# Performance work log

Measured on AMD Instinct MI355X. Metric: run time of the kernel, lower is better.

The kernel has to match this reference:

```python
import jax, jax.numpy as jnp
import numpy as np

# MX microscaling decode helpers. Codes are stored as int32 holding uint8 bit patterns.
_FP4_MAG = jnp.array([0.0, 0.5, 1.0, 1.5, 2.0, 3.0, 4.0, 6.0], dtype=jnp.float32)  # E2M1

def dec_fp4(c):
    # c in [0,16): bit3 = sign, bits0-2 index E2M1 magnitude LUT
    s = jnp.where(c >= 8, -1.0, 1.0)
    return s * _FP4_MAG[c & 7]

def dec_fp6(c):
    # E3M2, bias 3. bit5 sign, bits2-4 exp, bits0-1 mantissa
    s = jnp.where(c >= 32, -1.0, 1.0)
    e = ((c >> 2) & 7).astype(jnp.float32)
    m = (c & 3).astype(jnp.float32)
    mag = jnp.where(e == 0, m * 0.25 * 0.25, (1.0 + m * 0.25) * jnp.exp2(e - 3.0))
    return s * mag

def dec_fp8(c):
    # E4M3, bias 7. bit7 sign, bits3-6 exp, bits0-2 mantissa (NaN code decoded as 480, consistent both sides)
    s = jnp.where(c >= 128, -1.0, 1.0)
    e = ((c >> 3) & 15).astype(jnp.float32)
    m = (c & 7).astype(jnp.float32)
    mag = jnp.where(e == 0, m * 0.125 * jnp.exp2(-6.0), (1.0 + m * 0.125) * jnp.exp2(e - 7.0))
    return s * mag

def unpack4(p):
    # [..., K//2] bytes -> [..., K] nibbles; low nibble = even element, high = odd
    lo = p & 15
    hi = (p >> 4) & 15
    return jnp.stack([lo, hi], axis=-1).reshape(*p.shape[:-1], p.shape[-1] * 2)

def unpack6(p):
    # little-endian 6-bit packing: 4 values per 3 bytes. [..., K*6//8] -> [..., K]
    g = p.reshape(*p.shape[:-1], -1, 3)
    b0, b1, b2 = g[..., 0], g[..., 1], g[..., 2]
    v0 = b0 & 0x3F
    v1 = ((b0 >> 6) & 3) | ((b1 & 0x0F) << 2)
    v2 = ((b1 >> 4) & 0x0F) | ((b2 & 3) << 4)
    v3 = (b2 >> 2) & 0x3F
    return jnp.stack([v0, v1, v2, v3], axis=-1).reshape(*p.shape[:-1], p.shape[-1] * 4 // 3)

def blockscale(x, sf):
    # x [..., K] fp32, sf [..., K//32] E8M0 exponents: scale = 2^(sf-127) per 32-element block
    scale = jnp.exp2(sf.astype(jnp.float32) - 127.0)
    xs = x.reshape(*x.shape[:-1], -1, 32) * scale[..., None]
    return xs.reshape(x.shape)

def dequant(codes, sf, bits):
    if bits == 4:
        x = dec_fp4(unpack4(codes))
    elif bits == 6:
        x = dec_fp6(unpack6(codes))
    else:
        x = dec_fp8(codes)
    return blockscale(x, sf)


def setup_inputs() -> dict:
    key = jax.random.key(0)
    ks = jax.random.split(key, 13)
    M, N = 4096, 4096
    p4, p6, p8 = 3072, 768, 256
    ri = lambda k, sh: jax.random.randint(k, sh, 0, 256, dtype=jnp.int32)
    sf = lambda k, sh: jax.random.randint(k, sh, 121, 132, dtype=jnp.int32)
    return {
        "AN": ri(ks[0], (M, p4 // 2)),
        "AS": ri(ks[1], (M, p6 * 6 // 8)),
        "AO": ri(ks[2], (M, p8)),
        "SFAN": sf(ks[3], (M, p4 // 32)),
        "SFAS": sf(ks[4], (M, p6 // 32)),
        "SFAO": sf(ks[5], (M, p8 // 32)),
        "BN": ri(ks[6], (N, p4 // 2)),
        "BS": ri(ks[7], (N, p6 * 6 // 8)),
        "BO": ri(ks[8], (N, p8)),
        "SFBN": sf(ks[9], (N * p4 // 32,)),
        "SFBS": sf(ks[10], (N * p6 // 32,)),
        "SFBO": sf(ks[11], (N * p8 // 32,)),
        "bias": jax.random.normal(ks[12], (N,), dtype=jnp.float32) * 0.02,
    }


def reference(AN, AS, AO, SFAN, SFAS, SFAO, BN, BS, BO, SFBN, SFBS, SFBO, bias):
    N = BN.shape[0]
    a4 = dequant(AN, SFAN, 4)                       # [M, p4]
    w4 = dequant(BN, SFBN.reshape(N, -1), 4)        # [N, p4]
    a6 = dequant(AS, SFAS, 6)                       # [M, p6]
    w6 = dequant(BS, SFBS.reshape(N, -1), 6)        # [N, p6]
    a8 = dequant(AO, SFAO, 8)                       # [M, p8]
    w8 = dequant(BO, SFBO.reshape(N, -1), 8)        # [N, p8]
    y = a4 @ w4.T + a6 @ w6.T + a8 @ w8.T           # [M, N]
    return y + bias
```

## Files before the change

### kernel.cpp

```cpp
#include <hip/hip_runtime.h>

typedef short short8 __attribute__((ext_vector_type(8)));
typedef int   intx8  __attribute__((ext_vector_type(8)));
typedef float floatx16 __attribute__((ext_vector_type(16)));

__device__ __forceinline__ unsigned short f2bf(float f) {
    union { float f; unsigned u; } v; v.f = f;
    unsigned r = (v.u + 0x7FFF + ((v.u >> 16) & 1)) >> 16;
    return (unsigned short)r;
}
__device__ __forceinline__ float dec8f(int c) {
    float s = (c & 128) ? -1.f : 1.f;
    int e = (c >> 3) & 15, m = c & 7;
    float mag = e ? ldexpf(1.f + 0.125f * (float)m, e - 7) : ldexpf(0.125f * (float)m, -6);
    return s * mag;
}
__device__ __forceinline__ unsigned pk4(int a, int b, int c, int d) {
    return (a & 255) | ((b & 255) << 8) | ((c & 255) << 16) | ((unsigned)(d & 255) << 24);
}

__global__ __launch_bounds__(256) void pack_side(
    const int* __restrict__ Pn, const int* __restrict__ Ps, const int* __restrict__ Po,
    const int* __restrict__ Sn, const int* __restrict__ Ss, const int* __restrict__ So,
    unsigned char* __restrict__ C4, unsigned char* __restrict__ C6,
    unsigned short* __restrict__ C8, unsigned char* __restrict__ St, int R)
{
    int t = blockIdx.x * 256 + threadIdx.x;
    int T0 = R * 96, T1 = T0 + R * 24, T2 = T1 + R * 32, T3 = T2 + R * 24, T4 = T3 + R * 12;
    if (t < T0) {
        int j = t / R, r = t - j * R;
        const int4* p = (const int4*)(Pn + (size_t)r * 1536 + j * 16);
        uint4 o; unsigned* po = (unsigned*)&o;
        #pragma unroll
        for (int q = 0; q < 4; q++) { int4 b = p[q]; po[q] = pk4(b.x, b.y, b.z, b.w); }
        *(uint4*)(C4 + ((size_t)j * R + r) * 16) = o;
    } else if (t < T1) {
        t -= T0; int g = t / R, r = t - g * R;
        const int4* p = (const int4*)(Ps + (size_t)r * 576 + g * 24);
        unsigned d[6];
        #pragma unroll
        for (int q = 0; q < 6; q++) { int4 b = p[q]; d[q] = pk4(b.x, b.y, b.z, b.w); }
        unsigned char* dst = C6 + ((size_t)g * R + r) * 24;
        *(int2*)(dst)      = (int2){ (int)d[0], (int)d[1] };
        *(int2*)(dst + 8)  = (int2){ (int)d[2], (int)d[3] };
        *(int2*)(dst + 16) = (int2){ (int)d[4], (int)d[5] };
    } else if (t < T2) {
        t -= T1; int j = t / R, r = t - j * R;
        const int4* p = (const int4*)(Po + (size_t)r * 256 + j * 8);
        int4 c0 = p[0], c1 = p[1];
        int e = So[r * 8 + (j >> 2)] - 127;
        int cs[8] = { c0.x, c0.y, c0.z, c0.w, c1.x, c1.y, c1.z, c1.w };
        uint4 o; unsigned* po = (unsigned*)&o;
        #pragma unroll
        for (int i = 0; i < 4; i++) {
            unsigned lo = f2bf(ldexpf(dec8f(cs[2 * i] & 255), e));
            unsigned hi = f2bf(ldexpf(dec8f(cs[2 * i + 1] & 255), e));
            po[i] = lo | (hi << 16);
        }
        *(uint4*)((unsigned char*)C8 + ((size_t)j * R + r) * 16) = o;
    } else if (t < T3) {
        t -= T2; int q = t / R, r = t - q * R;
        int4 v = *(const int4*)(Sn + (size_t)r * 96 + q * 4);
        *(unsigned*)(St + ((size_t)q * R + r) * 4) = pk4(v.x, v.y, v.z, v.w);
    } else if (t < T4) {
        t -= T3; int b2 = t / R, r = t - b2 * R;
        int s0 = Ss[(size_t)r * 24 + 2 * b2] & 255, s1 = Ss[(size_t)r * 24 + 2 * b2 + 1] & 255;
        *(unsigned*)(St + ((size_t)(24 + b2) * R + r) * 4) = (unsigned)(s0 | (s1 << 8));
    }
}

__global__ __launch_bounds__(256, 2) void gemm_mx(
    const unsigned char* __restrict__ A4, const unsigned char* __restrict__ B4,
    const unsigned char* __restrict__ A6, const unsigned char* __restrict__ B6,
    const unsigned short* __restrict__ A8, const unsigned short* __restrict__ B8,
    const unsigned char* __restrict__ SaT, const unsigned char* __restrict__ SbT,
    const float* __restrict__ bias, float* __restrict__ C, int M, int N)
{
    int tid = threadIdx.x, w = tid >> 6, l = tid & 63;
    int bm = blockIdx.y, bn = blockIdx.x;
    int wm = (w >> 1) * 64, wn = (w & 1) * 64;
    int lr = l & 31, lh = l >> 5;

    floatx16 acc[2][2] = {};

    int rA[2] = { bm * 128 + wm + lr, bm * 128 + wm + 32 + lr };
    int cB[2] = { bn * 128 + wn + lr, bn * 128 + wn + 32 + lr };

    {
        unsigned offA[2] = { ((unsigned)lh * M + rA[0]) * 16u, ((unsigned)lh * M + rA[1]) * 16u };
        unsigned offB[2] = { ((unsigned)lh * N + cB[0]) * 16u, ((unsigned)lh * N + cB[1]) * 16u };
        unsigned strA = 32u * (unsigned)M, strB = 32u * (unsigned)N;
        #pragma unroll 2
        for (int up = 0; up < 24; ++up) {
            unsigned sca0 = *(const unsigned*)(SaT + ((size_t)up * M + rA[0]) * 4);
            unsigned sca1 = *(const unsigned*)(SaT + ((size_t)up * M + rA[1]) * 4);
            unsigned scb0 = *(const unsigned*)(SbT + ((size_t)up * N + cB[0]) * 4);
            unsigned scb1 = *(const unsigned*)(SbT + ((size_t)up * N + cB[1]) * 4);
            #pragma unroll
            for (int s = 0; s < 2; ++s) {
                unsigned u = (unsigned)(up * 2 + s);
                intx8 af[2], bfr[2];
                #pragma unroll
                for (int i = 0; i < 2; i++) {
                    int4 v = *(const int4*)(A4 + offA[i] + (size_t)u * strA);
                    af[i] = (intx8){ v.x, v.y, v.z, v.w, 0, 0, 0, 0 };
                }
                #pragma unroll
                for (int j = 0; j < 2; j++) {
                    int4 v = *(const int4*)(B4 + offB[j] + (size_t)u * strB);
                    bfr[j] = (intx8){ v.x, v.y, v.z, v.w, 0, 0, 0, 0 };
                }
                int sh = 8 * (s * 2 + lh);
                int sa[2] = { (int)((sca0 >> sh) & 255), (int)((sca1 >> sh) & 255) };
                int sb[2] = { (int)((scb0 >> sh) & 255), (int)((scb1 >> sh) & 255) };
                #pragma unroll
                for (int i = 0; i < 2; i++)
                    #pragma unroll
                    for (int j = 0; j < 2; j++)
                        acc[i][j] = __builtin_amdgcn_mfma_scale_f32_32x32x64_f8f6f4(
                            af[i], bfr[j], acc[i][j], 4, 4, 0, sa[i], 0, sb[j]);
            }
        }
    }

    {
        #pragma unroll 2
        for (int v = 0; v < 12; ++v) {
            unsigned sca0 = *(const unsigned*)(SaT + ((size_t)(24 + v) * M + rA[0]) * 4);
            unsigned sca1 = *(const unsigned*)(SaT + ((size_t)(24 + v) * M + rA[1]) * 4);
            unsigned scb0 = *(const unsigned*)(SbT + ((size_t)(24 + v) * N + cB[0]) * 4);
            unsigned scb1 = *(const unsigned*)(SbT + ((size_t)(24 + v) * N + cB[1]) * 4);
            intx8 af[2], bfr[2];
            #pragma unroll
            for (int i = 0; i < 2; i++) {
                const unsigned char* p = A6 + ((size_t)(2 * v + lh) * M + rA[i]) * 24;
                int2 u0 = *(const int2*)(p), u1 = *(const int2*)(p + 8), u2 = *(const int2*)(p + 16);
                af[i] = (intx8){ u0.x, u0.y, u1.x, u1.y, u2.x, u2.y, 0, 0 };
            }
            #pragma unroll
            for (int j = 0; j < 2; j++) {
                const unsigned char* p = B6 + ((size_t)(2 * v + lh) * N + cB[j]) * 24;
                int2 u0 = *(const int2*)(p), u1 = *(const int2*)(p + 8), u2 = *(const int2*)(p + 16);
                bfr[j] = (intx8){ u0.x, u0.y, u1.x, u1.y, u2.x, u2.y, 0, 0 };
            }
            int sh = 8 * lh;
            int sa[2] = { (int)((sca0 >> sh) & 255), (int)((sca1 >> sh) & 255) };
            int sb[2] = { (int)((scb0 >> sh) & 255), (int)((scb1 >> sh) & 255) };
            #pragma unroll
            for (int i = 0; i < 2; i++)
                #pragma unroll
                for (int j = 0; j < 2; j++)
                    acc[i][j] = __builtin_amdgcn_mfma_scale_f32_32x32x64_f8f6f4(
                        af[i], bfr[j], acc[i][j], 3, 3, 0, sa[i], 0, sb[j]);
        }
    }

    {
        #pragma unroll 2
        for (int q = 0; q < 16; ++q) {
            short8 af[2], bfr[2];
            #pragma unroll
            for (int i = 0; i < 2; i++)
                af[i] = *(const short8*)(A8 + ((size_t)(2 * q + lh) * M + rA[i]) * 8);
            #pragma unroll
            for (int j = 0; j < 2; j++)
                bfr[j] = *(const short8*)(B8 + ((size_t)(2 * q + lh) * N + cB[j]) * 8);
            #pragma unroll
            for (int i = 0; i < 2; i++)
                #pragma unroll
                for (int j = 0; j < 2; j++)
                    acc[i][j] = __builtin_amdgcn_mfma_f32_32x32x16_bf16(af[i], bfr[j], acc[i][j], 0, 0, 0);
        }
    }

    #pragma unroll
    for (int i = 0; i < 2; i++)
        #pragma unroll
        for (int j = 0; j < 2; j++) {
            int col = bn * 128 + wn + j * 32 + lr;
            float bv = bias[col];
            #pragma unroll
            for (int r = 0; r < 16; r++) {
                int row = bm * 128 + wm + i * 32 + (r & 3) + 8 * (r >> 2) + 4 * lh;
                C[(size_t)row * N + col] = acc[i][j][r] + bv;
            }
        }
}

extern "C" void kernel_launch(void* const* d_in, const int* in_sizes, int n_in,
                              void* d_out, int out_size, void* d_ws, size_t ws_size,
                              hipStream_t stream) {
    const int* AN   = (const int*)d_in[0];
    const int* ASs  = (const int*)d_in[1];
    const int* AO   = (const int*)d_in[2];
    const int* SFAN = (const int*)d_in[3];
    const int* SFAS = (const int*)d_in[4];
    const int* SFAO = (const int*)d_in[5];
    const int* BN   = (const int*)d_in[6];
    const int* BS   = (const int*)d_in[7];
    const int* BO   = (const int*)d_in[8];
    const int* SFBN = (const int*)d_in[9];
    const int* SFBS = (const int*)d_in[10];
    const int* SFBO = (const int*)d_in[11];
    const float* bias = (const float*)d_in[12];

    int M = in_sizes[0] / 1536;
    int N = in_sizes[6] / 1536;

    unsigned char* ws = (unsigned char*)d_ws;
    size_t o = 0;
    unsigned char*  A4c = ws + o;                    o += (size_t)M * 1536;
    unsigned char*  B4c = ws + o;                    o += (size_t)N * 1536;
    unsigned char*  A6c = ws + o;                    o += (size_t)M * 576;
    unsigned char*  B6c = ws + o;                    o += (size_t)N * 576;
    unsigned short* A8d = (unsigned short*)(ws + o); o += (size_t)M * 512;
    unsigned short* B8d = (unsigned short*)(ws + o); o += (size_t)N * 512;
    unsigned char*  SaT = ws + o;                    o += (size_t)36 * M * 4;
    unsigned char*  SbT = ws + o;                    o += (size_t)36 * N * 4;

    int TA = M * 188, TB = N * 188;
    pack_side<<<(TA + 255) / 256, 256, 0, stream>>>(AN, ASs, AO, SFAN, SFAS, SFAO,
                                                    A4c, A6c, A8d, SaT, M);
    pack_side<<<(TB + 255) / 256, 256, 0, stream>>>(BN, BS, BO, SFBN, SFBS, SFBO,
                                                    B4c, B6c, B8d, SbT, N);

    dim3 grid(N / 128, M / 128);
    gemm_mx<<<grid, 256, 0, stream>>>(A4c, B4c, A6c, B6c, A8d, B8d,
                                      SaT, SbT, bias, (float*)d_out, M, N);
}
```

Measured before the change: 227.6 us.

## Merge pack kernels, use integer fp8-to-bf16 decode, register-prefetch GEMM operands

The two pack launches are merged into one kernel, and each pack thread now handles more work. The fp8 decode to bf16 is rewritten as integer bit manipulation instead of float ldexp plus rounding. In the GEMM, every section (fp4, fp6, bf16) gets register double or quad buffering of operand fragments and scales, so global loads for later steps are issued before the current MFMAs run. This is meant to hide load latency in a kernel that does no LDS staging, at the cost of higher register pressure. That pressure could limit occupancy under launch_bounds(256,2).

New measurement: 209.9 us. 1.08x faster.

```diff
diff --git a/kernel.cpp b/kernel.cpp
--- a/kernel.cpp
+++ b/kernel.cpp
@@ -4,36 +4,36 @@
 typedef int   intx8  __attribute__((ext_vector_type(8)));
 typedef float floatx16 __attribute__((ext_vector_type(16)));
 
-__device__ __forceinline__ unsigned short f2bf(float f) {
-    union { float f; unsigned u; } v; v.f = f;
-    unsigned r = (v.u + 0x7FFF + ((v.u >> 16) & 1)) >> 16;
-    return (unsigned short)r;
-}
-__device__ __forceinline__ float dec8f(int c) {
-    float s = (c & 128) ? -1.f : 1.f;
-    int e = (c >> 3) & 15, m = c & 7;
-    float mag = e ? ldexpf(1.f + 0.125f * (float)m, e - 7) : ldexpf(0.125f * (float)m, -6);
-    return s * mag;
-}
 __device__ __forceinline__ unsigned pk4(int a, int b, int c, int d) {
     return (a & 255) | ((b & 255) << 8) | ((c & 255) << 16) | ((unsigned)(d & 255) << 24);
 }
 
-__global__ __launch_bounds__(256) void pack_side(
-    const int* __restrict__ Pn, const int* __restrict__ Ps, const int* __restrict__ Po,
+__device__ __forceinline__ unsigned dec8bf(int c, int esf) {
+    int s = (c & 128) << 8;
+    int e = (c >> 3) & 15, m = c & 7;
+    int rn = s | ((e + 120 + esf) << 7) | (m << 4);
+    int nb = (m >= 4) ? 2 : ((m >= 2) ? 1 : 0);
+    int rs = m ? (s | ((nb + 118 + esf) << 7) | ((m << (7 - nb)) & 0x7F)) : s;
+    return (unsigned)(e ? rn : rs);
+}
+
+__device__ __forceinline__ void pack_one(
+    int t, const int* __restrict__ Pn, const int* __restrict__ Ps, const int* __restrict__ Po,
     const int* __restrict__ Sn, const int* __restrict__ Ss, const int* __restrict__ So,
     unsigned char* __restrict__ C4, unsigned char* __restrict__ C6,
     unsigned short* __restrict__ C8, unsigned char* __restrict__ St, int R)
 {
-    int t = blockIdx.x * 256 + threadIdx.x;
-    int T0 = R * 96, T1 = T0 + R * 24, T2 = T1 + R * 32, T3 = T2 + R * 24, T4 = T3 + R * 12;
+    int T0 = R * 48, T1 = T0 + R * 24, T2 = T1 + R * 8, T3 = T2 + R * 24, T4 = T3 + R * 12;
     if (t < T0) {
-        int j = t / R, r = t - j * R;
-        const int4* p = (const int4*)(Pn + (size_t)r * 1536 + j * 16);
-        uint4 o; unsigned* po = (unsigned*)&o;
-        #pragma unroll
-        for (int q = 0; q < 4; q++) { int4 b = p[q]; po[q] = pk4(b.x, b.y, b.z, b.w); }
-        *(uint4*)(C4 + ((size_t)j * R + r) * 16) = o;
+        int jj = t / R, r = t - jj * R;
+        const int4* p = (const int4*)(Pn + (size_t)r * 1536 + jj * 32);
+        #pragma unroll
+        for (int h = 0; h < 2; ++h) {
+            uint4 o; unsigned* po = (unsigned*)&o;
+            #pragma unroll
+            for (int q = 0; q < 4; q++) { int4 b = p[4 * h + q]; po[q] = pk4(b.x, b.y, b.z, b.w); }
+            *(uint4*)(C4 + ((size_t)(2 * jj + h) * R + r) * 16) = o;
+        }
     } else if (t < T1) {
         t -= T0; int g = t / R, r = t - g * R;
         const int4* p = (const int4*)(Ps + (size_t)r * 576 + g * 24);
@@ -45,19 +45,19 @@
         *(int2*)(dst + 8)  = (int2){ (int)d[2], (int)d[3] };
         *(int2*)(dst + 16) = (int2){ (int)d[4], (int)d[5] };
     } else if (t < T2) {
-        t -= T1; int j = t / R, r = t - j * R;
-        const int4* p = (const int4*)(Po + (size_t)r * 256 + j * 8);
-        int4 c0 = p[0], c1 = p[1];
-        int e = So[r * 8 + (j >> 2)] - 127;
-        int cs[8] = { c0.x, c0.y, c0.z, c0.w, c1.x, c1.y, c1.z, c1.w };
-        uint4 o; unsigned* po = (unsigned*)&o;
-        #pragma unroll
-        for (int i = 0; i < 4; i++) {
-            unsigned lo = f2bf(ldexpf(dec8f(cs[2 * i] & 255), e));
-            unsigned hi = f2bf(ldexpf(dec8f(cs[2 * i + 1] & 255), e));
-            po[i] = lo | (hi << 16);
-        }
-        *(uint4*)((unsigned char*)C8 + ((size_t)j * R + r) * 16) = o;
+        t -= T1; int jj = t / R, r = t - jj * R;
+        const int4* p = (const int4*)(Po + (size_t)r * 256 + jj * 32);
+        int e = So[r * 8 + jj] - 127;
+        #pragma unroll
+        for (int cq = 0; cq < 4; ++cq) {
+            int4 c0 = p[2 * cq], c1 = p[2 * cq + 1];
+            int cs[8] = { c0.x, c0.y, c0.z, c0.w, c1.x, c1.y, c1.z, c1.w };
+            uint4 o; unsigned* po = (unsigned*)&o;
+            #pragma unroll
+            for (int i = 0; i < 4; i++)
+                po[i] = dec8bf(cs[2 * i] & 255, e) | (dec8bf(cs[2 * i + 1] & 255, e) << 16);
+            *(uint4*)((unsigned char*)C8 + ((size_t)(4 * jj + cq) * R + r) * 16) = o;
+        }
     } else if (t < T3) {
         t -= T2; int q = t / R, r = t - q * R;
         int4 v = *(const int4*)(Sn + (size_t)r * 96 + q * 4);
@@ -67,6 +67,22 @@
         int s0 = Ss[(size_t)r * 24 + 2 * b2] & 255, s1 = Ss[(size_t)r * 24 + 2 * b2 + 1] & 255;
         *(unsigned*)(St + ((size_t)(24 + b2) * R + r) * 4) = (unsigned)(s0 | (s1 << 8));
     }
+}
+
+__global__ __launch_bounds__(256) void pack_both(
+    const int* __restrict__ AN, const int* __restrict__ AS, const int* __restrict__ AO,
+    const int* __restrict__ SAn, const int* __restrict__ SAs, const int* __restrict__ SAo,
+    unsigned char* __restrict__ A4, unsigned char* __restrict__ A6,
+    unsigned short* __restrict__ A8, unsigned char* __restrict__ SaT, int M,
+    const int* __restrict__ BN, const int* __restrict__ BS, const int* __restrict__ BO,
+    const int* __restrict__ SBn, const int* __restrict__ SBs, const int* __restrict__ SBo,
+    unsigned char* __restrict__ B4, unsigned char* __restrict__ B6,
+    unsigned short* __restrict__ B8, unsigned char* __restrict__ SbT, int N)
+{
+    int t = blockIdx.x * 256 + threadIdx.x;
+    int TA = M * 116;
+    if (t < TA) pack_one(t, AN, AS, AO, SAn, SAs, SAo, A4, A6, A8, SaT, M);
+    else        pack_one(t - TA, BN, BS, BO, SBn, SBs, SBo, B4, B6, B8, SbT, N);
 }
 
 __global__ __launch_bounds__(256, 2) void gemm_mx(
@@ -87,89 +103,148 @@
     int cB[2] = { bn * 128 + wn + lr, bn * 128 + wn + 32 + lr };
 
     {
-        unsigned offA[2] = { ((unsigned)lh * M + rA[0]) * 16u, ((unsigned)lh * M + rA[1]) * 16u };
-        unsigned offB[2] = { ((unsigned)lh * N + cB[0]) * 16u, ((unsigned)lh * N + cB[1]) * 16u };
         unsigned strA = 32u * (unsigned)M, strB = 32u * (unsigned)N;
+        unsigned fA0 = ((unsigned)lh * M + (unsigned)rA[0]) * 16u;
+        unsigned fA1 = ((unsigned)lh * M + (unsigned)rA[1]) * 16u;
+        unsigned fB0 = ((unsigned)lh * N + (unsigned)cB[0]) * 16u;
+        unsigned fB1 = ((unsigned)lh * N + (unsigned)cB[1]) * 16u;
+
+        int4 pa[4][2], pb[4][2];
+        #pragma unroll
+        for (int s = 0; s < 4; ++s) {
+            pa[s][0] = *(const int4*)(A4 + fA0); pa[s][1] = *(const int4*)(A4 + fA1);
+            pb[s][0] = *(const int4*)(B4 + fB0); pb[s][1] = *(const int4*)(B4 + fB1);
+            fA0 += strA; fA1 += strA; fB0 += strB; fB1 += strB;
+        }
+
+        unsigned sstrA = 4u * (unsigned)M, sstrB = 4u * (unsigned)N;
+        unsigned sA0 = (unsigned)rA[0] * 4u, sA1 = (unsigned)rA[1] * 4u;
+        unsigned sB0 = (unsigned)cB[0] * 4u, sB1 = (unsigned)cB[1] * 4u;
+        unsigned psa[2][2], psb[2][2];
+        psa[0][0] = *(const unsigned*)(SaT + sA0);         psa[0][1] = *(const unsigned*)(SaT + sA1);
+        psb[0][0] = *(const unsigned*)(SbT + sB0);         psb[0][1] = *(const unsigned*)(SbT + sB1);
+        psa[1][0] = *(const unsigned*)(SaT + sA0 + sstrA); psa[1][1] = *(const unsigned*)(SaT + sA1 + sstrA);
+        psb[1][0] = *(const unsigned*)(SbT + sB0 + sstrB); psb[1][1] = *(const unsigned*)(SbT + sB1 + sstrB);
+        sA0 += 2 * sstrA; sA1 += 2 * sstrA; sB0 += 2 * sstrB; sB1 += 2 * sstrB;
+
+        #pragma unroll 4
+        for (int u = 0; u < 48; ++u) {
+            int sl = u & 3, wsl = (u >> 1) & 1;
+            int sh = 8 * ((u & 1) * 2 + lh);
+            int sa0 = (int)((psa[wsl][0] >> sh) & 255), sa1 = (int)((psa[wsl][1] >> sh) & 255);
+            int sb0 = (int)((psb[wsl][0] >> sh) & 255), sb1 = (int)((psb[wsl][1] >> sh) & 255);
+            intx8 A0 = (intx8){ pa[sl][0].x, pa[sl][0].y, pa[sl][0].z, pa[sl][0].w, 0, 0, 0, 0 };
+            intx8 A1 = (intx8){ pa[sl][1].x, pa[sl][1].y, pa[sl][1].z, pa[sl][1].w, 0, 0, 0, 0 };
+            intx8 B0 = (intx8){ pb[sl][0].x, pb[sl][0].y, pb[sl][0].z, pb[sl][0].w, 0, 0, 0, 0 };
+            intx8 B1 = (intx8){ pb[sl][1].x, pb[sl][1].y, pb[sl][1].z, pb[sl][1].w, 0, 0, 0, 0 };
+            acc[0][0] = __builtin_amdgcn_mfma_scale_f32_32x32x64_f8f6f4(A0, B0, acc[0][0], 4, 4, 0, sa0, 0, sb0);
+            acc[0][1] = __builtin_amdgcn_mfma_scale_f32_32x32x64_f8f6f4(A0, B1, acc[0][1], 4, 4, 0, sa0, 0, sb1);
+            acc[1][0] = __builtin_amdgcn_mfma_scale_f32_32x32x64_f8f6f4(A1, B0, acc[1][0], 4, 4, 0, sa1, 0, sb0);
+            acc[1][1] = __builtin_amdgcn_mfma_scale_f32_32x32x64_f8f6f4(A1, B1, acc[1][1], 4, 4, 0, sa1, 0, sb1);
+            pa[sl][0] = *(const int4*)(A4 + fA0); pa[sl][1] = *(const int4*)(A4 + fA1);
+            pb[sl][0] = *(const int4*)(B4 + fB0); pb[sl][1] = *(const int4*)(B4 + fB1);
+            fA0 += strA; fA1 += strA; fB0 += strB; fB1 += strB;
+            if (u & 1) {
+                psa[wsl][0] = *(const unsigned*)(SaT + sA0); psa[wsl][1] = *(const unsigned*)(SaT + sA1);
+                psb[wsl][0] = *(const unsigned*)(SbT + sB0); psb[wsl][1] = *(const unsigned*)(SbT + sB1);
+                sA0 += sstrA; sA1 += sstrA; sB0 += sstrB; sB1 += sstrB;
+            }
+        }
+    }
+
+    {
+        unsigned str6A = 48u * (unsigned)M, str6B = 48u * (unsigned)N;
+        unsigned gA0 = ((unsigned)lh * M + (unsigned)rA[0]) * 24u;
+        unsigned gA1 = ((unsigned)lh * M + (unsigned)rA[1]) * 24u;
+        unsigned gB0 = ((unsigned)lh * N + (unsigned)cB[0]) * 24u;
+        unsigned gB1 = ((unsigned)lh * N + (unsigned)cB[1]) * 24u;
+        unsigned ss4A = 4u * (unsigned)M, ss4B = 4u * (unsigned)N;
+        unsigned zA0 = (24u * (unsigned)M + (unsigned)rA[0]) * 4u;
+        unsigned zA1 = (24u * (unsigned)M + (unsigned)rA[1]) * 4u;
+        unsigned zB0 = (24u * (unsigned)N + (unsigned)cB[0]) * 4u;
+        unsigned zB1 = (24u * (unsigned)N + (unsigned)cB[1]) * 4u;
+
+        int2 qa[2][2][3], qb[2][2][3];
+        unsigned p6a[2][2], p6b[2][2];
+        #pragma unroll
+        for (int s = 0; s < 2; ++s) {
+            const unsigned char *a0 = A6 + gA0, *a1 = A6 + gA1, *b0 = B6 + gB0, *b1 = B6 + gB1;
+            qa[s][0][0] = *(const int2*)(a0); qa[s][0][1] = *(const int2*)(a0 + 8); qa[s][0][2] = *(const int2*)(a0 + 16);
+            qa[s][1][0] = *(const int2*)(a1); qa[s][1][1] = *(const int2*)(a1 + 8); qa[s][1][2] = *(const int2*)(a1 + 16);
+            qb[s][0][0] = *(const int2*)(b0); qb[s][0][1] = *(const int2*)(b0 + 8); qb[s][0][2] = *(const int2*)(b0 + 16);
+            qb[s][1][0] = *(const int2*)(b1); qb[s][1][1] = *(const int2*)(b1 + 8); qb[s][1][2] = *(const int2*)(b1 + 16);
+            p6a[s][0] = *(const unsigned*)(SaT + zA0); p6a[s][1] = *(const unsigned*)(SaT + zA1);
+            p6b[s][0] = *(const unsigned*)(SbT + zB0); p6b[s][1] = *(const unsigned*)(SbT + zB1);
+            gA0 += str6A; gA1 += str6A; gB0 += str6B; gB1 += str6B;
+            zA0 += ss4A; zA1 += ss4A; zB0 += ss4B; zB1 += ss4B;
+        }
+        int sh6 = 8 * lh;
         #pragma unroll 2
-        for (int up = 0; up < 24; ++up) {
-            unsigned sca0 = *(const unsigned*)(SaT + ((size_t)up * M + rA[0]) * 4);
-            unsigned sca1 = *(const unsigned*)(SaT + ((size_t)up * M + rA[1]) * 4);
-            unsigned scb0 = *(const unsigned*)(SbT + ((size_t)up * N + cB[0]) * 4);
-            unsigned scb1 = *(const unsigned*)(SbT + ((size_t)up * N + cB[1]) * 4);
-            #pragma unroll
-            for (int s = 0; s < 2; ++s) {
-                unsigned u = (unsigned)(up * 2 + s);
-                intx8 af[2], bfr[2];
-                #pragma unroll
-                for (int i = 0; i < 2; i++) {
-                    int4 v = *(const int4*)(A4 + offA[i] + (size_t)u * strA);
-                    af[i] = (intx8){ v.x, v.y, v.z, v.w, 0, 0, 0, 0 };
-                }
-                #pragma unroll
-                for (int j = 0; j < 2; j++) {
-                    int4 v = *(const int4*)(B4 + offB[j] + (size_t)u * strB);
-                    bfr[j] = (intx8){ v.x, v.y, v.z, v.w, 0, 0, 0, 0 };
-                }
-                int sh = 8 * (s * 2 + lh);
-                int sa[2] = { (int)((sca0 >> sh) & 255), (int)((sca1 >> sh) & 255) };
-                int sb[2] = { (int)((scb0 >> sh) & 255), (int)((scb1 >> sh) & 255) };
-                #pragma unroll
-                for (int i = 0; i < 2; i++)
-                    #pragma unroll
-                    for (int j = 0; j < 2; j++)
-                        acc[i][j] = __builtin_amdgcn_mfma_scale_f32_32x32x64_f8f6f4(
-                            af[i], bfr[j], acc[i][j], 4, 4, 0, sa[i], 0, sb[j]);
+        for (int v = 0; v < 10; ++v) {
+            int sl = v & 1;
+            int sa0 = (int)((p6a[sl][0] >> sh6) & 255), sa1 = (int)((p6a[sl][1] >> sh6) & 255);
+            int sb0 = (int)((p6b[sl][0] >> sh6) & 255), sb1 = (int)((p6b[sl][1] >> sh6) & 255);
+            intx8 A0 = (intx8){ qa[sl][0][0].x, qa[sl][0][0].y, qa[sl][0][1].x, qa[sl][0][1].y, qa[sl][0][2].x, qa[sl][0][2].y, 0, 0 };
+            intx8 A1 = (intx8){ qa[sl][1][0].x, qa[sl][1][0].y, qa[sl][1][1].x, qa[sl][1][1].y, qa[sl][1][2].x, qa[sl][1][2].y, 0, 0 };
+            intx8 B0 = (intx8){ qb[sl][0][0].x, qb[sl][0][0].y, qb[sl][0][1].x, qb[sl][0][1].y, qb[sl][0][2].x, qb[sl][0][2].y, 0, 0 };
+            intx8 B1 = (intx8){ qb[sl][1][0].x, qb[sl][1][0].y, qb[sl][1][1].x, qb[sl][1][1].y, qb[sl][1][2].x, qb[sl][1][2].y, 0, 0 };
+            acc[0][0] = __builtin_amdgcn_mfma_scale_f32_32x32x64_f8f6f4(A0, B0, acc[0][0], 3, 3, 0, sa0, 0, sb0);
+            acc[0][1] = __builtin_amdgcn_mfma_scale_f32_32x32x64_f8f6f4(A0, B1, acc[0][1], 3, 3, 0, sa0, 0, sb1);
+            acc[1][0] = __builtin_amdgcn_mfma_scale_f32_32x32x64_f8f6f4(A1, B0, acc[1][0], 3, 3, 0, sa1, 0, sb0);
+            acc[1][1] = __builtin_amdgcn_mfma_scale_f32_32x32x64_f8f6f4(A1, B1, acc[1][1], 3, 3, 0, sa1, 0, sb1);
+            {
+                const unsigned char *a0 = A6 + gA0, *a1 = A6 + gA1, *b0 = B6 + gB0, *b1 = B6 + gB1;
+                qa[sl][0][0] = *(const int2*)(a0); qa[sl][0][1] = *(const int2*)(a0 + 8); qa[sl][0][2] = *(const int2*)(a0 + 16);
+                qa[sl][1][0] = *(const int2*)(a1); qa[sl][1][1] = *(const int2*)(a1 + 8); qa[sl][1][2] = *(const int2*)(a1 + 16);
+                qb[sl][0][0] = *(const int2*)(b0); qb[sl][0][1] = *(const int2*)(b0 + 8); qb[sl][0][2] = *(const int2*)(b0 + 16);
+                qb[sl][1][0] = *(const int2*)(b1); qb[sl][1][1] = *(const int2*)(b1 + 8); qb[sl][1][2] = *(const int2*)(b1 + 16);
+                p6a[sl][0] = *(const unsigned*)(SaT + zA0); p6a[sl][1] = *(const unsigned*)(SaT + zA1);
+                p6b[sl][0] = *(const unsigned*)(SbT + zB0); p6b[sl][1] = *(const unsigned*)(SbT + zB1);
+                gA0 += str6A; gA1 += str6A; gB0 += str6B; gB1 += str6B;
+                zA0 += ss4A; zA1 += ss4A; zB0 += ss4B; zB1 += ss4B;
             }
         }
+        #pragma unroll
+        for (int v = 10; v < 12; ++v) {
+            int sl = v & 1;
+            int sa0 = (int)((p6a[sl][0] >> sh6) & 255), sa1 = (int)((p6a[sl][1] >> sh6) & 255);
+            int sb0 = (int)((p6b[sl][0] >> sh6) & 255), sb1 = (int)((p6b[sl][1] >> sh6) & 255);
+            intx8 A0 = (intx8){ qa[sl][0][0].x, qa[sl][0][0].y, qa[sl][0][1].x, qa[sl][0][1].y, qa[sl][0][2].x, qa[sl][0][2].y, 0, 0 };
+            intx8 A1 = (intx8){ qa[sl][1][0].x, qa[sl][1][0].y, qa[sl][1][1].x, qa[sl][1][1].y, qa[sl][1][2].x, qa[sl][1][2].y, 0, 0 };
+            intx8 B0 = (intx8){ qb[sl][0][0].x, qb[sl][0][0].y, qb[sl][0][1].x, qb[sl][0][1].y, qb[sl][0][2].x, qb[sl][0][2].y, 0, 0 };
+            intx8 B1 = (intx8){ qb[sl][1][0].x, qb[sl][1][0].y, qb[sl][1][1].x, qb[sl][1][1].y, qb[sl][1][2].x, qb[sl][1][2].y, 0, 0 };
+            acc[0][0] = __builtin_amdgcn_mfma_scale_f32_32x32x64_f8f6f4(A0, B0, acc[0][0], 3, 3, 0, sa0, 0, sb0);
+            acc[0][1] = __builtin_amdgcn_mfma_scale_f32_32x32x64_f8f6f4(A0, B1, acc[0][1], 3, 3, 0, sa0, 0, sb1);
+            acc[1][0] = __builtin_amdgcn_mfma_scale_f32_32x32x64_f8f6f4(A1, B0, acc[1][0], 3, 3, 0, sa1, 0, sb0);
+            acc[1][1] = __builtin_amdgcn_mfma_scale_f32_32x32x64_f8f6f4(A1, B1, acc[1][1], 3, 3, 0, sa1, 0, sb1);
+        }
     }
 
     {
-        #pragma unroll 2
-        for (int v = 0; v < 12; ++v) {
-            unsigned sca0 = *(const unsigned*)(SaT + ((size_t)(24 + v) * M + rA[0]) * 4);
-            unsigned sca1 = *(const unsigned*)(SaT + ((size_t)(24 + v) * M + rA[1]) * 4);
-            unsigned scb0 = *(const unsigned*)(SbT + ((size_t)(24 + v) * N + cB[0]) * 4);
-            unsigned scb1 = *(const unsigned*)(SbT + ((size_t)(24 + v) * N + cB[1]) * 4);
-            intx8 af[2], bfr[2];
-            #pragma unroll
-            for (int i = 0; i < 2; i++) {
-                const unsigned char* p = A6 + ((size_t)(2 * v + lh) * M + rA[i]) * 24;
-                int2 u0 = *(const int2*)(p), u1 = *(const int2*)(p + 8), u2 = *(const int2*)(p + 16);
-                af[i] = (intx8){ u0.x, u0.y, u1.x, u1.y, u2.x, u2.y, 0, 0 };
-            }
-            #pragma unroll
-            for (int j = 0; j < 2; j++) {
-                const unsigned char* p = B6 + ((size_t)(2 * v + lh) * N + cB[j]) * 24;
-                int2 u0 = *(const int2*)(p), u1 = *(const int2*)(p + 8), u2 = *(const int2*)(p + 16);
-                bfr[j] = (intx8){ u0.x, u0.y, u1.x, u1.y, u2.x, u2.y, 0, 0 };
-            }
-            int sh = 8 * lh;
-            int sa[2] = { (int)((sca0 >> sh) & 255), (int)((sca1 >> sh) & 255) };
-            int sb[2] = { (int)((scb0 >> sh) & 255), (int)((scb1 >> sh) & 255) };
-            #pragma unroll
-            for (int i = 0; i < 2; i++)
-                #pragma unroll
-                for (int j = 0; j < 2; j++)
-                    acc[i][j] = __builtin_amdgcn_mfma_scale_f32_32x32x64_f8f6f4(
-                        af[i], bfr[j], acc[i][j], 3, 3, 0, sa[i], 0, sb[j]);
-        }
-    }
-
-    {
+        unsigned str8A = 32u * (unsigned)M, str8B = 32u * (unsigned)N;
+        const unsigned char* A8b = (const unsigned char*)A8;
+        const unsigned char* B8b = (const unsigned char*)B8;
+        unsigned hA0 = ((unsigned)lh * M + (unsigned)rA[0]) * 16u;
+        unsigned hA1 = ((unsigned)lh * M + (unsigned)rA[1]) * 16u;
+        unsigned hB0 = ((unsigned)lh * N + (unsigned)cB[0]) * 16u;
+        unsigned hB1 = ((unsigned)lh * N + (unsigned)cB[1]) * 16u;
+        short8 ra[2][2], rb[2][2];
+        #pragma unroll
+        for (int s = 0; s < 2; ++s) {
+            ra[s][0] = *(const short8*)(A8b + hA0); ra[s][1] = *(const short8*)(A8b + hA1);
+            rb[s][0] = *(const short8*)(B8b + hB0); rb[s][1] = *(const short8*)(B8b + hB1);
+            hA0 += str8A; hA1 += str8A; hB0 += str8B; hB1 += str8B;
+        }
         #pragma unroll 2
         for (int q = 0; q < 16; ++q) {
-            short8 af[2], bfr[2];
-            #pragma unroll
-            for (int i = 0; i < 2; i++)
-                af[i] = *(const short8*)(A8 + ((size_t)(2 * q + lh) * M + rA[i]) * 8);
-            #pragma unroll
-            for (int j = 0; j < 2; j++)
-                bfr[j] = *(const short8*)(B8 + ((size_t)(2 * q + lh) * N + cB[j]) * 8);
-            #pragma unroll
-            for (int i = 0; i < 2; i++)
-                #pragma unroll
-                for (int j = 0; j < 2; j++)
-                    acc[i][j] = __builtin_amdgcn_mfma_f32_32x32x16_bf16(af[i], bfr[j], acc[i][j], 0, 0, 0);
+            int sl = q & 1;
+            acc[0][0] = __builtin_amdgcn_mfma_f32_32x32x16_bf16(ra[sl][0], rb[sl][0], acc[0][0], 0, 0, 0);
+            acc[0][1] = __builtin_amdgcn_mfma_f32_32x32x16_bf16(ra[sl][0], rb[sl][1], acc[0][1], 0, 0, 0);
+            acc[1][0] = __builtin_amdgcn_mfma_f32_32x32x16_bf16(ra[sl][1], rb[sl][0], acc[1][0], 0, 0, 0);
+            acc[1][1] = __builtin_amdgcn_mfma_f32_32x32x16_bf16(ra[sl][1], rb[sl][1], acc[1][1], 0, 0, 0);
+            ra[sl][0] = *(const short8*)(A8b + hA0); ra[sl][1] = *(const short8*)(A8b + hA1);
+            rb[sl][0] = *(const short8*)(B8b + hB0); rb[sl][1] = *(const short8*)(B8b + hB1);
+            hA0 += str8A; hA1 += str8A; hB0 += str8B; hB1 += str8B;
         }
     }
 
@@ -218,11 +293,10 @@
     unsigned char*  SaT = ws + o;                    o += (size_t)36 * M * 4;
     unsigned char*  SbT = ws + o;                    o += (size_t)36 * N * 4;
 
-    int TA = M * 188, TB = N * 188;
-    pack_side<<<(TA + 255) / 256, 256, 0, stream>>>(AN, ASs, AO, SFAN, SFAS, SFAO,
-                                                    A4c, A6c, A8d, SaT, M);
-    pack_side<<<(TB + 255) / 256, 256, 0, stream>>>(BN, BS, BO, SFBN, SFBS, SFBO,
-                                                    B4c, B6c, B8d, SbT, N);
+    int T = M * 116 + N * 116;
+    pack_both<<<(T + 255) / 256, 256, 0, stream>>>(
+        AN, ASs, AO, SFAN, SFAS, SFAO, A4c, A6c, A8d, SaT, M,
+        BN, BS, BO, SFBN, SFBS, SFBO, B4c, B6c, B8d, SbT, N);
 
     dim3 grid(N / 128, M / 128);
     gemm_mx<<<grid, 256, 0, stream>>>(A4c, B4c, A6c, B6c, A8d, B8d,
```
